# Kernel optimization log

Hardware: AMD Instinct MI355X
Metric: run time of the kernel (lower is better)

Reference implementation:

```python
import jax, jax.numpy as jnp
import numpy as np

T, B, S = 64, 32, 128
E, Q, H = 512, 512, 256  # src_encoding_size, query_vec_size, hidden_dim


def setup_inputs() -> dict:
    key = jax.random.key(0)
    ks = jax.random.split(key, 9)
    return {
        "src_encodings": jax.random.normal(ks[0], (B, S, E), jnp.float32),
        "src_token_mask": jax.random.randint(ks[1], (B, S), 0, 2).astype(bool),
        "query_vec": jax.random.normal(ks[2], (T, B, Q), jnp.float32),
        # learned params (nn.Linear stores W as (out, in))
        "W_src": jax.random.normal(ks[3], (H, E), jnp.float32) * (1.0 / np.sqrt(E)),
        "b_src": jax.random.normal(ks[4], (H,), jnp.float32) * 0.01,
        "W_q": jax.random.normal(ks[5], (H, Q), jnp.float32) * (1.0 / np.sqrt(Q)),
        "b_q": jax.random.normal(ks[6], (H,), jnp.float32) * 0.01,
        "w2": jax.random.normal(ks[7], (H,), jnp.float32) * (1.0 / np.sqrt(H)),
        "b2": jax.random.normal(ks[8], (), jnp.float32) * 0.01,
    }


def reference(src_encodings, src_token_mask, query_vec, W_src, b_src, W_q, b_q, w2, b2):
    # src projection: (B,S,H); query projection: (T,B,H)
    src_proj = jnp.einsum('bse,he->bsh', src_encodings, W_src) + b_src
    q_proj = jnp.einsum('tbq,hq->tbh', query_vec, W_q) + b_q
    # broadcast add -> tanh: (T,B,S,H)
    h1 = jnp.tanh(src_proj[None, :, :, :] + q_proj[:, :, None, :])
    # hidden -> 1 reduction: (T,B,S)
    h2 = jnp.einsum('tbsh,h->tbs', h1, w2) + b2
    h2 = jnp.where(src_token_mask[None, :, :], -jnp.inf, h2)
    return jax.nn.softmax(h2, axis=-1)
```

## Files before the change

### kernel.cpp

```cpp
#include <hip/hip_runtime.h>
#include <hip/hip_bf16.h>
#include <math.h>


#define TANH_PRESCALE 2.8853900817779268f
#define LOG2E        1.4426950408889634f

typedef __attribute__((ext_vector_type(8))) short short8;
typedef __attribute__((ext_vector_type(4))) float f32x4;

__device__ __forceinline__ float fast_exp2(float x) {
#if __has_builtin(__builtin_amdgcn_exp2f)
    return __builtin_amdgcn_exp2f(x);
#else
    return exp2f(x);
#endif
}
__device__ __forceinline__ float fast_rcp(float x) {
#if __has_builtin(__builtin_amdgcn_rcpf)
    return __builtin_amdgcn_rcpf(x);
#else
    return 1.0f / x;
#endif
}
__device__ __forceinline__ float hi_part(float x) {
    return __uint_as_float(__float_as_uint(x) & 0xffff0000u);
}
__device__ __forceinline__ unsigned pack2(float a, float b) {
    return __builtin_amdgcn_perm(__float_as_uint(b), __float_as_uint(a), 0x07060302u);
}

#define AHI 0
#define ALO 4608
#define WHI 9216
#define WLO 13824
#define LDS_USH 18432

__global__ __launch_bounds__(256) void proj_gemm(
    const float* __restrict__ src, const float* __restrict__ query,
    const float* __restrict__ Wsrc, const float* __restrict__ Wq,
    const float* __restrict__ b_src, const float* __restrict__ b_q,
    float* __restrict__ spq, float* __restrict__ qp)
{
    const int bx = blockIdx.x;
    const int nb = blockIdx.y;
    const bool isSrc = bx < 64;
    const int mrow0 = (isSrc ? bx : bx - 64) * 64;
    const float* __restrict__ A    = isSrc ? src  : query;
    const float* __restrict__ W    = isSrc ? Wsrc : Wq;
    const float* __restrict__ bias = isSrc ? b_src : b_q;

    __shared__ unsigned short LS[LDS_USH];

    const int tid  = threadIdx.x;
    const int lane = tid & 63;
    const int wv   = tid >> 6;
    const int wm   = wv & 1, wn = wv >> 1;
    const int l15  = lane & 15;
    const int q4   = lane >> 4;

    const int srow = tid >> 3;
    const int sc8  = tid & 7;

    f32x4 acc[2][2];
    #pragma unroll
    for (int i = 0; i < 2; ++i)
        #pragma unroll
        for (int j = 0; j < 2; ++j) acc[i][j] = (f32x4){0.f, 0.f, 0.f, 0.f};

    const float* Ab = A + (size_t)mrow0 * 512 + sc8 * 8;
    const float* Wb = W + (size_t)(nb * 64) * 512 + sc8 * 8;

    for (int kt = 0; kt < 512; kt += 64) {
        __syncthreads();
        #pragma unroll
        for (int p = 0; p < 2; ++p) {
            const int row = srow + 32 * p;
            const float* g = Ab + (size_t)row * 512 + kt;
            float4 v0 = *(const float4*)g, v1 = *(const float4*)(g + 4);
            uint4 h; uint4 l;
            h.x = pack2(v0.x, v0.y);  h.y = pack2(v0.z, v0.w);
            h.z = pack2(v1.x, v1.y);  h.w = pack2(v1.z, v1.w);
            l.x = pack2(v0.x - hi_part(v0.x), v0.y - hi_part(v0.y));
            l.y = pack2(v0.z - hi_part(v0.z), v0.w - hi_part(v0.w));
            l.z = pack2(v1.x - hi_part(v1.x), v1.y - hi_part(v1.y));
            l.w = pack2(v1.z - hi_part(v1.z), v1.w - hi_part(v1.w));
            *(uint4*)&LS[AHI + row * 72 + sc8 * 8] = h;
            *(uint4*)&LS[ALO + row * 72 + sc8 * 8] = l;
        }
        #pragma unroll
        for (int p = 0; p < 2; ++p) {
            const int row = srow + 32 * p;
            const float* g = Wb + (size_t)row * 512 + kt;
            float4 v0 = *(const float4*)g, v1 = *(const float4*)(g + 4);
            uint4 h; uint4 l;
            h.x = pack2(v0.x, v0.y);  h.y = pack2(v0.z, v0.w);
            h.z = pack2(v1.x, v1.y);  h.w = pack2(v1.z, v1.w);
            l.x = pack2(v0.x - hi_part(v0.x), v0.y - hi_part(v0.y));
            l.y = pack2(v0.z - hi_part(v0.z), v0.w - hi_part(v0.w));
            l.z = pack2(v1.x - hi_part(v1.x), v1.y - hi_part(v1.y));
            l.w = pack2(v1.z - hi_part(v1.z), v1.w - hi_part(v1.w));
            *(uint4*)&LS[WHI + row * 72 + sc8 * 8] = h;
            *(uint4*)&LS[WLO + row * 72 + sc8 * 8] = l;
        }
        __syncthreads();

        #pragma unroll
        for (int pass = 0; pass < 3; ++pass) {
            const unsigned short* Ap = LS + (pass == 2 ? ALO : AHI);
            const unsigned short* Wp = LS + (pass == 1 ? WLO : WHI);
            #pragma unroll
            for (int kk = 0; kk < 2; ++kk) {
                const int off = (kk * 4 + q4) * 8;
                short8 a0 = *(const short8*)&Ap[(wm * 32 + l15)      * 72 + off];
                short8 a1 = *(const short8*)&Ap[(wm * 32 + 16 + l15) * 72 + off];
                short8 w0 = *(const short8*)&Wp[(wn * 32 + l15)      * 72 + off];
                short8 w1 = *(const short8*)&Wp[(wn * 32 + 16 + l15) * 72 + off];
                acc[0][0] = __builtin_amdgcn_mfma_f32_16x16x32_bf16(a0, w0, acc[0][0], 0, 0, 0);
                acc[0][1] = __builtin_amdgcn_mfma_f32_16x16x32_bf16(a0, w1, acc[0][1], 0, 0, 0);
                acc[1][0] = __builtin_amdgcn_mfma_f32_16x16x32_bf16(a1, w0, acc[1][0], 0, 0, 0);
                acc[1][1] = __builtin_amdgcn_mfma_f32_16x16x32_bf16(a1, w1, acc[1][1], 0, 0, 0);
            }
        }
    }

    float bl[2];
    #pragma unroll
    for (int ni = 0; ni < 2; ++ni)
        bl[ni] = bias[nb * 64 + wn * 32 + ni * 16 + l15];

    __syncthreads();
    float* E = (float*)LS;
    #pragma unroll
    for (int mi = 0; mi < 2; ++mi)
        #pragma unroll
        for (int ni = 0; ni < 2; ++ni) {
            const int m = wm * 32 + mi * 16 + q4 * 4;
            const int n = wn * 32 + ni * 16 + l15;
            #pragma unroll
            for (int r = 0; r < 4; ++r)
                E[(m + r) * 68 + n] =
                    fast_exp2((acc[mi][ni][r] + bl[ni]) * TANH_PRESCALE);
        }
    __syncthreads();

    if (isSrc) {
        const int nq = tid >> 4;
        #pragma unroll
        for (int j = 0; j < 4; ++j) {
            const int m = (tid & 15) + 16 * j;
            float4 v = *(const float4*)&E[m * 68 + nq * 4];
            *(float4*)(spq + (size_t)(nb * 16 + nq) * 16384
                           + (size_t)(mrow0 + m) * 4) = v;
        }
    } else {
        #pragma unroll
        for (int p = 0; p < 4; ++p) {
            const int idx = p * 256 + tid;
            const int m = idx >> 4, c4 = idx & 15;
            float4 v = *(const float4*)&E[m * 68 + c4 * 4];
            *(float4*)(qp + (size_t)(mrow0 + m) * 256 + nb * 64 + c4 * 4) = v;
        }
    }
}

__global__ __launch_bounds__(512) void attn_score(
    const float* __restrict__ spq, const float* __restrict__ qp,
    const float* __restrict__ w2, const int* __restrict__ mask,
    float* __restrict__ out)
{
    const int b  = blockIdx.x;
    const int tz = blockIdx.y;
    const int tid = threadIdx.x;

    __shared__ float qp_s[4][256];
    __shared__ float w2_s[256];
    __shared__ float h2p[4][4][128];

    int mk0 = 0, mk1 = 0;
    if (tid < 256) {
        const int tl = tid >> 6, lane = tid & 63;
        const int t = tz * 4 + tl;
        *(float4*)&qp_s[tl][lane * 4] =
            *(const float4*)(qp + (size_t)(t * 32 + b) * 256 + lane * 4);
        mk0 = mask[b * 128 + lane];
        mk1 = mask[b * 128 + lane + 64];
    } else if (tid < 320) {
        const int i = tid - 256;
        *(float4*)&w2_s[i * 4] = *(const float4*)(w2 + i * 4);
    }
    __syncthreads();

    const int s = tid & 127;
    const int g = tid >> 7;
    const int hb = g * 64;
    const float* sq = spq + (size_t)(g * 16) * 16384 + (size_t)(b * 128 + s) * 4;

    float acc0 = 0.f, acc1 = 0.f, acc2 = 0.f, acc3 = 0.f;
    float4 s4 = *(const float4*)sq;
    #pragma unroll 4
    for (int hq = 0; hq < 16; ++hq) {
        float4 nxt;
        if (hq < 15) nxt = *(const float4*)(sq + (size_t)(hq + 1) * 16384);
        float4 w4 = *(const float4*)&w2_s[hb + hq * 4];
        float4 q0 = *(const float4*)&qp_s[0][hb + hq * 4];
        float4 q1 = *(const float4*)&qp_s[1][hb + hq * 4];
        float4 q2 = *(const float4*)&qp_s[2][hb + hq * 4];
        float4 q3 = *(const float4*)&qp_s[3][hb + hq * 4];
        #define PN_TERM(sj, wj, q0j, q1j, q2j, q3j)                              \
            { float r;                                                           \
              r = fast_rcp(fmaf(sj, q0j, 1.0f)); acc0 = fmaf(wj, r, acc0);       \
              r = fast_rcp(fmaf(sj, q1j, 1.0f)); acc1 = fmaf(wj, r, acc1);       \
              r = fast_rcp(fmaf(sj, q2j, 1.0f)); acc2 = fmaf(wj, r, acc2);       \
              r = fast_rcp(fmaf(sj, q3j, 1.0f)); acc3 = fmaf(wj, r, acc3); }
        PN_TERM(s4.x, w4.x, q0.x, q1.x, q2.x, q3.x)
        PN_TERM(s4.y, w4.y, q0.y, q1.y, q2.y, q3.y)
        PN_TERM(s4.z, w4.z, q0.z, q1.z, q2.z, q3.z)
        PN_TERM(s4.w, w4.w, q0.w, q1.w, q2.w, q3.w)
        #undef PN_TERM
        s4 = nxt;
    }
    h2p[g][0][s] = acc0;
    h2p[g][1][s] = acc1;
    h2p[g][2][s] = acc2;
    h2p[g][3][s] = acc3;
    __syncthreads();

    if (tid < 256) {
        const int wv = tid >> 6, lane = tid & 63;
        float v0 = -2.0f * (h2p[0][wv][lane] + h2p[1][wv][lane]
                          + h2p[2][wv][lane] + h2p[3][wv][lane]);
        float v1 = -2.0f * (h2p[0][wv][lane + 64] + h2p[1][wv][lane + 64]
                          + h2p[2][wv][lane + 64] + h2p[3][wv][lane + 64]);
        if (mk0) v0 = -__builtin_inff();
        if (mk1) v1 = -__builtin_inff();

        float mx = fmaxf(v0, v1);
        #pragma unroll
        for (int off = 32; off >= 1; off >>= 1) mx = fmaxf(mx, __shfl_xor(mx, off));
        float e0 = fast_exp2((v0 - mx) * LOG2E);
        float e1 = fast_exp2((v1 - mx) * LOG2E);
        float sum = e0 + e1;
        #pragma unroll
        for (int off = 32; off >= 1; off >>= 1) sum += __shfl_xor(sum, off);
        const float r = fast_rcp(sum);

        const size_t ob = (size_t)((tz * 4 + wv) * 32 + b) * 128;
        out[ob + lane]      = e0 * r;
        out[ob + lane + 64] = e1 * r;
    }
}

extern "C" void kernel_launch(void* const* d_in, const int* in_sizes, int n_in,
                              void* d_out, int out_size, void* d_ws, size_t ws_size,
                              hipStream_t stream) {
    const float* src   = (const float*)d_in[0];
    const int*   mask  = (const int*)  d_in[1];
    const float* query = (const float*)d_in[2];
    const float* W_src = (const float*)d_in[3];
    const float* b_src = (const float*)d_in[4];
    const float* W_q   = (const float*)d_in[5];
    const float* b_q   = (const float*)d_in[6];
    const float* w2    = (const float*)d_in[7];
    float* out = (float*)d_out;

    float* spq = (float*)d_ws;
    float* qp  = (float*)((char*)d_ws + (4u << 20));

    proj_gemm<<<dim3(96, 4), 256, 0, stream>>>(src, query, W_src, W_q,
                                               b_src, b_q, spq, qp);
    attn_score<<<dim3(32, 16), 512, 0, stream>>>(spq, qp, w2, mask, out);
}
```

Before: 96.59 us.

## Compact unmasked source positions and pair reciprocals in attention scoring

Each block now builds a compacted list of unmasked source positions with a ballot and prefix popcount, so only threads mapped to kept positions run the tanh-sum loop. The compacted results are mapped back to their positions through an inverse index before the softmax. The inner loop also merges two reciprocals into one by summing w_a/d_a + w_b/d_b as a single fraction, halving the rcp count at the cost of extra multiplies and some overflow or precision risk. Masked positions still come out as -inf, so the output is unchanged, but work per block now depends on how many positions are masked.

```diff
diff --git a/kernel.cpp b/kernel.cpp
--- a/kernel.cpp
+++ b/kernel.cpp
@@ -176,64 +176,90 @@
     __shared__ float qp_s[4][256];
     __shared__ float w2_s[256];
     __shared__ float h2p[4][4][128];
-
-    int mk0 = 0, mk1 = 0;
+    __shared__ int   list_s[128];
+    __shared__ int   inv_s[128];
+    __shared__ int   cnt_s[2];
+    __shared__ int   nU_s;
+
+    int keep = 0, pre = 0, w01 = 0;
     if (tid < 256) {
         const int tl = tid >> 6, lane = tid & 63;
         const int t = tz * 4 + tl;
         *(float4*)&qp_s[tl][lane * 4] =
             *(const float4*)(qp + (size_t)(t * 32 + b) * 256 + lane * 4);
-        mk0 = mask[b * 128 + lane];
-        mk1 = mask[b * 128 + lane + 64];
     } else if (tid < 320) {
         const int i = tid - 256;
         *(float4*)&w2_s[i * 4] = *(const float4*)(w2 + i * 4);
     }
-    __syncthreads();
-
-    const int s = tid & 127;
-    const int g = tid >> 7;
+    if (tid < 128) {
+        w01  = tid >> 6;
+        keep = !mask[b * 128 + tid];
+        const unsigned long long bal = __ballot(keep);
+        pre  = __popcll(bal & ((1ull << (tid & 63)) - 1ull));
+        if ((tid & 63) == 0) cnt_s[w01] = (int)__popcll(bal);
+        inv_s[tid] = -1;
+    }
+    __syncthreads();
+    if (tid < 128 && keep) {
+        const int pos = (w01 ? cnt_s[0] : 0) + pre;
+        list_s[pos] = tid;
+        inv_s[tid]  = pos;
+    }
+    if (tid == 0) nU_s = cnt_s[0] + cnt_s[1];
+    __syncthreads();
+
+    const int j  = tid & 127;
+    const int g  = tid >> 7;
     const int hb = g * 64;
-    const float* sq = spq + (size_t)(g * 16) * 16384 + (size_t)(b * 128 + s) * 4;
-
-    float acc0 = 0.f, acc1 = 0.f, acc2 = 0.f, acc3 = 0.f;
-    float4 s4 = *(const float4*)sq;
-    #pragma unroll 4
-    for (int hq = 0; hq < 16; ++hq) {
-        float4 nxt;
-        if (hq < 15) nxt = *(const float4*)(sq + (size_t)(hq + 1) * 16384);
-        float4 w4 = *(const float4*)&w2_s[hb + hq * 4];
-        float4 q0 = *(const float4*)&qp_s[0][hb + hq * 4];
-        float4 q1 = *(const float4*)&qp_s[1][hb + hq * 4];
-        float4 q2 = *(const float4*)&qp_s[2][hb + hq * 4];
-        float4 q3 = *(const float4*)&qp_s[3][hb + hq * 4];
-        #define PN_TERM(sj, wj, q0j, q1j, q2j, q3j)                              \
-            { float r;                                                           \
-              r = fast_rcp(fmaf(sj, q0j, 1.0f)); acc0 = fmaf(wj, r, acc0);       \
-              r = fast_rcp(fmaf(sj, q1j, 1.0f)); acc1 = fmaf(wj, r, acc1);       \
-              r = fast_rcp(fmaf(sj, q2j, 1.0f)); acc2 = fmaf(wj, r, acc2);       \
-              r = fast_rcp(fmaf(sj, q3j, 1.0f)); acc3 = fmaf(wj, r, acc3); }
-        PN_TERM(s4.x, w4.x, q0.x, q1.x, q2.x, q3.x)
-        PN_TERM(s4.y, w4.y, q0.y, q1.y, q2.y, q3.y)
-        PN_TERM(s4.z, w4.z, q0.z, q1.z, q2.z, q3.z)
-        PN_TERM(s4.w, w4.w, q0.w, q1.w, q2.w, q3.w)
-        #undef PN_TERM
-        s4 = nxt;
-    }
-    h2p[g][0][s] = acc0;
-    h2p[g][1][s] = acc1;
-    h2p[g][2][s] = acc2;
-    h2p[g][3][s] = acc3;
+    const int nU = nU_s;
+
+    if (j < nU) {
+        const int s = list_s[j];
+        const float* sq = spq + (size_t)(g * 16) * 16384
+                              + (size_t)(b * 128 + s) * 4;
+
+        float acc0 = 0.f, acc1 = 0.f, acc2 = 0.f, acc3 = 0.f;
+        float4 s4 = *(const float4*)sq;
+        #pragma unroll 4
+        for (int hq = 0; hq < 16; ++hq) {
+            float4 nxt;
+            if (hq < 15) nxt = *(const float4*)(sq + (size_t)(hq + 1) * 16384);
+            float4 w4 = *(const float4*)&w2_s[hb + hq * 4];
+            float4 q0 = *(const float4*)&qp_s[0][hb + hq * 4];
+            float4 q1 = *(const float4*)&qp_s[1][hb + hq * 4];
+            float4 q2 = *(const float4*)&qp_s[2][hb + hq * 4];
+            float4 q3 = *(const float4*)&qp_s[3][hb + hq * 4];
+            #define PN_PAIR(sa, sb, wa, wb, qa, qb, accv)                     \
+                { float da = fmaf(sa, qa, 1.0f);                              \
+                  float db = fmaf(sb, qb, 1.0f);                              \
+                  float nm = fmaf(wa, db, wb * da);                           \
+                  accv = fmaf(nm, fast_rcp(da * db), accv); }
+            PN_PAIR(s4.x, s4.y, w4.x, w4.y, q0.x, q0.y, acc0)
+            PN_PAIR(s4.x, s4.y, w4.x, w4.y, q1.x, q1.y, acc1)
+            PN_PAIR(s4.x, s4.y, w4.x, w4.y, q2.x, q2.y, acc2)
+            PN_PAIR(s4.x, s4.y, w4.x, w4.y, q3.x, q3.y, acc3)
+            PN_PAIR(s4.z, s4.w, w4.z, w4.w, q0.z, q0.w, acc0)
+            PN_PAIR(s4.z, s4.w, w4.z, w4.w, q1.z, q1.w, acc1)
+            PN_PAIR(s4.z, s4.w, w4.z, w4.w, q2.z, q2.w, acc2)
+            PN_PAIR(s4.z, s4.w, w4.z, w4.w, q3.z, q3.w, acc3)
+            #undef PN_PAIR
+            s4 = nxt;
+        }
+        h2p[g][0][j] = acc0;
+        h2p[g][1][j] = acc1;
+        h2p[g][2][j] = acc2;
+        h2p[g][3][j] = acc3;
+    }
     __syncthreads();
 
     if (tid < 256) {
         const int wv = tid >> 6, lane = tid & 63;
-        float v0 = -2.0f * (h2p[0][wv][lane] + h2p[1][wv][lane]
-                          + h2p[2][wv][lane] + h2p[3][wv][lane]);
-        float v1 = -2.0f * (h2p[0][wv][lane + 64] + h2p[1][wv][lane + 64]
-                          + h2p[2][wv][lane + 64] + h2p[3][wv][lane + 64]);
-        if (mk0) v0 = -__builtin_inff();
-        if (mk1) v1 = -__builtin_inff();
+        const int j0 = inv_s[lane], j1 = inv_s[lane + 64];
+        float v0 = -__builtin_inff(), v1 = -__builtin_inff();
+        if (j0 >= 0) v0 = -2.0f * (h2p[0][wv][j0] + h2p[1][wv][j0]
+                                 + h2p[2][wv][j0] + h2p[3][wv][j0]);
+        if (j1 >= 0) v1 = -2.0f * (h2p[0][wv][j1] + h2p[1][wv][j1]
+                                 + h2p[2][wv][j1] + h2p[3][wv][j1]);
 
         float mx = fmaxf(v0, v1);
         #pragma unroll
```

Measured after the change: 96.18 us. About the same (-0.4%).
